# Kernel optimization log

Measured on AMD Instinct MI355X. Metric: run time of the kernel, lower is better.

The kernel has to match this reference:

```python
import jax, jax.numpy as jnp
import numpy as np

B, S, D = 4, 1024, 4096
HQ, HKV, HD = 32, 8, 128
N_REP = HQ // HKV


def _rope(x, cos, sin):
    # x: [b, s, h, hd]; cos/sin: [s, hd//2]; pairs are (x[..., 2i], x[..., 2i+1])
    xr = x[..., 0::2]
    xi = x[..., 1::2]
    c = cos[None, :, None, :]
    s = sin[None, :, None, :]
    out_r = xr * c - xi * s
    out_i = xr * s + xi * c
    return jnp.stack([out_r, out_i], axis=-1).reshape(x.shape)


def setup_inputs() -> dict:
    key = jax.random.key(0)
    ks = jax.random.split(key, 6)
    x = jax.random.normal(ks[0], (B, S, D), dtype=jnp.float32)
    wq = jax.random.normal(ks[1], (HQ * HD, D), dtype=jnp.float32) * 0.02
    wk = jax.random.normal(ks[2], (HKV * HD, D), dtype=jnp.float32) * 0.02
    wv = jax.random.normal(ks[3], (HKV * HD, D), dtype=jnp.float32) * 0.02
    wo = jax.random.normal(ks[4], (D, HQ * HD), dtype=jnp.float32) * 0.02
    # standard rotary frequencies, theta=10000
    inv_freq = 1.0 / (10000.0 ** (np.arange(0, HD, 2, dtype=np.float32) / HD))
    angles = np.outer(np.arange(S, dtype=np.float32), inv_freq)  # [S, HD//2]
    freqs_cos = jnp.asarray(np.cos(angles), dtype=jnp.float32)
    freqs_sin = jnp.asarray(np.sin(angles), dtype=jnp.float32)
    cache_k = jnp.zeros((B, S, HKV, HD), dtype=jnp.float32)
    cache_v = jnp.zeros((B, S, HKV, HD), dtype=jnp.float32)
    return {"x": x, "wq": wq, "wk": wk, "wv": wv, "wo": wo,
            "freqs_cos": freqs_cos, "freqs_sin": freqs_sin,
            "cache_k": cache_k, "cache_v": cache_v, "start_pos": 0}


def reference(x, wq, wk, wv, wo, freqs_cos, freqs_sin, cache_k, cache_v, start_pos):
    b, s, _ = x.shape
    xq = jnp.einsum('bsd,od->bso', x, wq).reshape(b, s, HQ, HD)
    xk = jnp.einsum('bsd,od->bso', x, wk).reshape(b, s, HKV, HD)
    xv = jnp.einsum('bsd,od->bso', x, wv).reshape(b, s, HKV, HD)
    xq = _rope(xq, freqs_cos, freqs_sin)
    xk = _rope(xk, freqs_cos, freqs_sin)
    # KV-cache append (intended semantics: store keys/values)
    cache_k = jax.lax.dynamic_update_slice(cache_k, xk, (0, start_pos, 0, 0))
    cache_v = jax.lax.dynamic_update_slice(cache_v, xv, (0, start_pos, 0, 0))
    keys = cache_k[:, :start_pos + s]      # [b, kv, HKV, HD]
    values = cache_v[:, :start_pos + s]
    # GQA repeat_kv -> [b, kv, HQ, HD]
    keys = jnp.repeat(keys, N_REP, axis=2)
    values = jnp.repeat(values, N_REP, axis=2)
    scores = jnp.einsum('bqhd,bkhd->bhqk', xq, keys) / jnp.sqrt(jnp.float32(HD))
    probs = jax.nn.softmax(scores.astype(jnp.float32), axis=-1).astype(xq.dtype)
    out = jnp.einsum('bhqk,bkhd->bqhd', probs, values).reshape(b, s, HQ * HD)
    return jnp.einsum('bso,do->bsd', out, wo)
```

## Files before the change

### kernel.cpp

```cpp
#include <hip/hip_runtime.h>

typedef __bf16 bf16_t;
typedef __bf16 bf16x8 __attribute__((ext_vector_type(8)));
typedef __bf16 bf16x4 __attribute__((ext_vector_type(4)));
typedef float  f32x4  __attribute__((ext_vector_type(4)));
typedef unsigned u32x4 __attribute__((ext_vector_type(4)));

#define SEQ    1024
#define DMODEL 4096
#define NHQ    32
#define NHKV   8
#define HDIM   128

#define GLOAD_LDS16(g, l)                                                  \
    __builtin_amdgcn_global_load_lds(                                      \
        (const __attribute__((address_space(1))) unsigned int*)(g),        \
        (__attribute__((address_space(3))) unsigned int*)(l), 16, 0, 0)

__global__ __launch_bounds__(256)
void f2b(const float* __restrict__ in, bf16_t* __restrict__ out, int n8)
{
    int i = blockIdx.x * 256 + threadIdx.x;
    if (i >= n8) return;
    const float4* p = (const float4*)in + 2 * (size_t)i;
    float4 a = p[0], b = p[1];
    bf16x8 o;
    o[0] = (bf16_t)a.x; o[1] = (bf16_t)a.y; o[2] = (bf16_t)a.z; o[3] = (bf16_t)a.w;
    o[4] = (bf16_t)b.x; o[5] = (bf16_t)b.y; o[6] = (bf16_t)b.z; o[7] = (bf16_t)b.w;
    *((bf16x8*)out + i) = o;
}

#define MFMA_(a, b, c) __builtin_amdgcn_mfma_f32_16x16x32_bf16(a, b, c, 0, 0, 0)
#define BAR    __builtin_amdgcn_s_barrier()
#define SCB    __builtin_amdgcn_sched_barrier(0)
#define PRIO1  __builtin_amdgcn_s_setprio(1)
#define PRIO0  __builtin_amdgcn_s_setprio(0)
#define WVM4   do { asm volatile("s_waitcnt vmcnt(4)" ::: "memory"); SCB; } while (0)

#define SA(bufo, half, ktb)  do {                                          \
    const char* g_ = ((half) ? aS1 : aS0) + (ktb);                         \
    GLOAD_LDS16(g_,      sd + (bufo) + (half) * 8192);                     \
    GLOAD_LDS16(g_ + 64, sd + (bufo) + (half) * 8192 + 16384);             \
} while (0)
#define SB(bufo, half, ktb)  do {                                          \
    const char* g_ = ((half) ? bS1 : bS0) + (ktb);                         \
    GLOAD_LDS16(g_,      sd + (bufo) + 32768 + (half) * 8192);             \
    GLOAD_LDS16(g_ + 64, sd + (bufo) + 32768 + (half) * 8192 + 16384);     \
} while (0)
#define LDA(bufo, mh) do { _Pragma("unroll")                               \
    for (int j = 0; j < 4; ++j) {                                          \
        afq[j][0] = *(const bf16x8*)(lds + (bufo) + aRow + (mh)*4096 + j*1024);         \
        afq[j][1] = *(const bf16x8*)(lds + (bufo) + aRow + (mh)*4096 + j*1024 + 16384); \
    } } while (0)
#define LDB(bufo, nh, dst) do { _Pragma("unroll")                          \
    for (int n2 = 0; n2 < 2; ++n2) {                                       \
        dst[n2][0] = *(const bf16x8*)(lds + (bufo) + bRow + (nh)*2048 + n2*1024);         \
        dst[n2][1] = *(const bf16x8*)(lds + (bufo) + bRow + (nh)*2048 + n2*1024 + 16384); \
    } } while (0)
#define MMQ(mlo, bfx, nlo) do { _Pragma("unroll")                          \
    for (int j = 0; j < 4; ++j) {                                          \
        acc[(mlo)+j][(nlo)  ] = MFMA_(afq[j][0], bfx[0][0], acc[(mlo)+j][(nlo)  ]); \
        acc[(mlo)+j][(nlo)  ] = MFMA_(afq[j][1], bfx[0][1], acc[(mlo)+j][(nlo)  ]); \
        acc[(mlo)+j][(nlo)+1] = MFMA_(afq[j][0], bfx[1][0], acc[(mlo)+j][(nlo)+1]); \
        acc[(mlo)+j][(nlo)+1] = MFMA_(afq[j][1], bfx[1][1], acc[(mlo)+j][(nlo)+1]); \
    } } while (0)

template<bool OUT_F32>
__global__ __launch_bounds__(512, 2)
void gemm256(const bf16_t* __restrict__ A, const bf16_t* __restrict__ B,
             void* __restrict__ Cv, int M, int N, int K, int nbn)
{
    __shared__ __align__(16) char lds[131072];

    const int nwg = gridDim.x;
    const int bid0 = blockIdx.x;
    const int bid = (bid0 & 7) * (nwg >> 3) + (bid0 >> 3);
    const int bm = bid / nbn, bn = bid % nbn;
    const int t = threadIdx.x;
    const int lane = t & 63, wid = t >> 6;
    const int wm = wid >> 2, wn = wid & 3;
    const int l15 = lane & 15, lg = lane >> 4;
    const int m0 = bm * 256, n0 = bn * 256;

    const int Krb = K * 2;
    const int srow = t >> 2;
    const int schunk = (((t & 3) ^ ((t >> 3) & 3)) << 4);
    const char* aS0 = (const char*)A + (size_t)(m0 + srow) * Krb + schunk;
    const char* aS1 = (const char*)A + (size_t)(m0 + 128 + srow) * Krb + schunk;
    const char* bS0 = (const char*)B + (size_t)(n0 + srow) * Krb + schunk;
    const char* bS1 = (const char*)B + (size_t)(n0 + 128 + srow) * Krb + schunk;
    char* sd = lds + t * 16;

    const int rchunk = ((lg ^ ((l15 >> 1) & 3)) << 4);
    const int aRow = (wm * 128 + l15) * 64 + rchunk;
    const int bRow = 32768 + (wn * 64 + l15) * 64 + rchunk;

    const int NT = K >> 6;
    f32x4 acc[8][4] = {};
    bf16x8 afq[4][2], bf0[2][2], bf1[2][2];

    SA(0, 0, 0); SA(0, 1, 0); SB(0, 0, 0); SB(0, 1, 0);
    SB(65536, 0, 128); SB(65536, 1, 128);
    WVM4;
    BAR;

    for (int T = 0; T < NT; T += 2) {
        const int k1 = (T + 1) * 128;
        const int k2 = (T + 2 < NT) ? (T + 2) * 128 : 0;
        const int k3 = (T + 3 < NT) ? (T + 3) * 128 : 0;
        LDA(0, 0); LDB(0, 0, bf0); SA(65536, 0, k1); BAR; SCB;
        PRIO1; MMQ(0, bf0, 0); PRIO0; BAR;
        LDB(0, 1, bf1); SA(65536, 1, k1); BAR; SCB;
        PRIO1; MMQ(0, bf1, 2); PRIO0; BAR;
        LDA(0, 1); SB(0, 0, k2); BAR; SCB;
        PRIO1; MMQ(4, bf1, 2); PRIO0; BAR;
        SB(0, 1, k2); BAR;
        PRIO1; MMQ(4, bf0, 0); PRIO0; WVM4; BAR;
        LDA(65536, 0); LDB(65536, 0, bf0); SA(0, 0, k2); BAR; SCB;
        PRIO1; MMQ(0, bf0, 0); PRIO0; BAR;
        LDB(65536, 1, bf1); SA(0, 1, k2); BAR; SCB;
        PRIO1; MMQ(0, bf1, 2); PRIO0; BAR;
        LDA(65536, 1); SB(65536, 0, k3); BAR; SCB;
        PRIO1; MMQ(4, bf1, 2); PRIO0; BAR;
        SB(65536, 1, k3); BAR;
        PRIO1; MMQ(4, bf0, 0); PRIO0; WVM4; BAR;
    }

    #pragma unroll
    for (int m = 0; m < 8; ++m) {
        int row0 = m0 + wm * 128 + m * 16 + lg * 4;
        #pragma unroll
        for (int n = 0; n < 4; ++n) {
            int col = n0 + wn * 64 + n * 16 + l15;
            #pragma unroll
            for (int i = 0; i < 4; ++i) {
                if constexpr (OUT_F32)
                    ((float*)Cv)[(size_t)(row0 + i) * N + col] = acc[m][n][i];
                else
                    ((bf16_t*)Cv)[(size_t)(row0 + i) * N + col] = (bf16_t)acc[m][n][i];
            }
        }
    }
}

template<int MODE>
__global__ __launch_bounds__(256, 4)
void gemm_bt(const bf16_t* __restrict__ A, const bf16_t* __restrict__ B,
             void* __restrict__ Cv, bf16_t* __restrict__ Vt,
             int M, int N, int K, int nbn)
{
    __shared__ __align__(16) bf16_t lA[128 * 32];
    __shared__ __align__(16) bf16_t lB[128 * 32];

    const int nwg = gridDim.x;
    const int bid0 = blockIdx.x;
    const int bid = (bid0 & 7) * (nwg >> 3) + (bid0 >> 3);
    const int bm = bid / nbn, bn = bid % nbn;
    const int t = threadIdx.x;
    const int lane = t & 63, wid = t >> 6;
    const int wrow = (wid >> 1) * 64, wcol = (wid & 1) * 64;
    const int l15 = lane & 15, lg = lane >> 4;
    const int m0 = bm * 128, n0 = bn * 128;

    const int r0 = t >> 2, pos0 = (t & 3) * 8;
    const int r1 = r0 + 64;

    const bf16_t* Ar0 = A + (size_t)(m0 + r0) * K + pos0;
    const bf16_t* Ar1 = A + (size_t)(m0 + r1) * K + pos0;
    const bf16_t* Br0 = B + (size_t)(n0 + r0) * K + pos0;
    const bf16_t* Br1 = B + (size_t)(n0 + r1) * K + pos0;

    f32x4 acc[4][4] = {};

    for (int k0 = 0; k0 < K; k0 += 32) {
        __syncthreads();
        GLOAD_LDS16(Ar0 + k0, lA + t * 8);
        GLOAD_LDS16(Ar1 + k0, lA + (t + 256) * 8);
        GLOAD_LDS16(Br0 + k0, lB + t * 8);
        GLOAD_LDS16(Br1 + k0, lB + (t + 256) * 8);
        __syncthreads();

        bf16x8 af[4], bfr[4];
        #pragma unroll
        for (int m = 0; m < 4; ++m)
            af[m] = *(const bf16x8*)(lA + (wrow + m * 16 + l15) * 32 + lg * 8);
        #pragma unroll
        for (int n = 0; n < 4; ++n)
            bfr[n] = *(const bf16x8*)(lB + (wcol + n * 16 + l15) * 32 + lg * 8);
        #pragma unroll
        for (int m = 0; m < 4; ++m)
            #pragma unroll
            for (int n = 0; n < 4; ++n)
                acc[m][n] = __builtin_amdgcn_mfma_f32_16x16x32_bf16(
                    af[m], bfr[n], acc[m][n], 0, 0, 0);
    }

    #pragma unroll
    for (int m = 0; m < 4; ++m) {
        #pragma unroll
        for (int n = 0; n < 4; ++n) {
            int col  = n0 + wcol + n * 16 + l15;
            int row0 = m0 + wrow + m * 16 + lg * 4;
            if constexpr (MODE == 0) {
                #pragma unroll
                for (int i = 0; i < 4; ++i)
                    ((bf16_t*)Cv)[(size_t)(row0 + i) * N + col] = (bf16_t)acc[m][n][i];
            } else if constexpr (MODE == 1) {
                #pragma unroll
                for (int i = 0; i < 4; ++i)
                    ((float*)Cv)[(size_t)(row0 + i) * N + col] = acc[m][n][i];
            } else {
                if (col < 1024) {
                    #pragma unroll
                    for (int i = 0; i < 4; ++i)
                        ((bf16_t*)Cv)[(size_t)(row0 + i) * 1024 + col] = (bf16_t)acc[m][n][i];
                } else {
                    bf16x4 pk;
                    #pragma unroll
                    for (int i = 0; i < 4; ++i) pk[i] = (bf16_t)acc[m][n][i];
                    *(bf16x4*)(Vt + (size_t)(col - 1024) * 4096 + row0) = pk;
                }
            }
        }
    }
}

__global__ __launch_bounds__(256)
void rope_kernel(bf16_t* __restrict__ X, const float* __restrict__ fc,
                 const float* __restrict__ fs, int nheads, int rowstride,
                 float oscale)
{
    int idx = blockIdx.x * 256 + threadIdx.x;
    int j4 = idx & 15;
    int rest = idx >> 4;
    int h = rest % nheads;
    int tok = rest / nheads;
    int s = tok & (SEQ - 1);
    bf16_t* p = X + (size_t)tok * rowstride + h * HDIM + j4 * 8;
    bf16x8 v = *(const bf16x8*)p;
    float4 c  = *(const float4*)(fc + s * 64 + j4 * 4);
    float4 sn = *(const float4*)(fs + s * 64 + j4 * 4);
    c.x *= oscale; c.y *= oscale; c.z *= oscale; c.w *= oscale;
    sn.x *= oscale; sn.y *= oscale; sn.z *= oscale; sn.w *= oscale;
    bf16x8 o;
    o[0] = (bf16_t)((float)v[0] * c.x - (float)v[1] * sn.x);
    o[1] = (bf16_t)((float)v[0] * sn.x + (float)v[1] * c.x);
    o[2] = (bf16_t)((float)v[2] * c.y - (float)v[3] * sn.y);
    o[3] = (bf16_t)((float)v[2] * sn.y + (float)v[3] * c.y);
    o[4] = (bf16_t)((float)v[4] * c.z - (float)v[5] * sn.z);
    o[5] = (bf16_t)((float)v[4] * sn.z + (float)v[5] * c.z);
    o[6] = (bf16_t)((float)v[6] * c.w - (float)v[7] * sn.w);
    o[7] = (bf16_t)((float)v[6] * sn.w + (float)v[7] * c.w);
    *(bf16x8*)p = o;
}

__global__ __launch_bounds__(512, 2)
void attn_kernel(const bf16_t* __restrict__ Q, const bf16_t* __restrict__ Kg,
                 const bf16_t* __restrict__ Vtg, bf16_t* __restrict__ O)
{
    __shared__ __align__(16) char klds[2][64 * 256];
    __shared__ __align__(16) char vlds[2][128 * 128];

    const int nwg = gridDim.x;
    const int bid0 = blockIdx.x;
    const int blk = (bid0 & 7) * (nwg >> 3) + (bid0 >> 3);
    const int qt = blk & 7;
    const int bh = blk >> 3;
    const int b = bh >> 5, h = bh & 31, kv = h >> 2;
    const int t = threadIdx.x, lane = t & 63, wid = t >> 6;
    const int l15 = lane & 15, lg = lane >> 4;
    const int swzk = (l15 & 7) << 4;

    const int qrow = qt * 128 + wid * 16 + l15;
    const size_t qbase = (size_t)(b * SEQ + qrow) * DMODEL + h * HDIM;
    bf16x8 qf[4];
    #pragma unroll
    for (int dc = 0; dc < 4; ++dc)
        qf[dc] = *(const bf16x8*)(Q + qbase + dc * 32 + lg * 8);

    const char* kgb = (const char*)Kg + ((size_t)(b * SEQ) * 1024 + kv * HDIM) * 2;
    const char* vgb = (const char*)Vtg + ((size_t)(kv * HDIM) * 4096 + b * SEQ) * 2;

    const int ck0 = t, ck1 = t + 512;
    const int kr0 = ck0 >> 4, kr1 = ck1 >> 4;
    const int kg0 = ((kr0 >> 5) << 5) + (((((kr0 & 15) >> 2) ^ ((kr0 >> 4) & 1)) << 3))
                  + (((kr0 >> 4) & 1) << 2) + (kr0 & 3);
    const int kg1 = ((kr1 >> 5) << 5) + (((((kr1 & 15) >> 2) ^ ((kr1 >> 4) & 1)) << 3))
                  + (((kr1 >> 4) & 1) << 2) + (kr1 & 3);
    const int kf0 = kg0 * 2048 + ((((ck0 & 15) << 4)) ^ ((kr0 & 7) << 4));
    const int kf1 = kg1 * 2048 + ((((ck1 & 15) << 4)) ^ ((kr1 & 7) << 4));
    const int vd0 = ck0 >> 3, vf0 = vd0 * 8192 + ((((ck0 & 7) << 4)) ^ ((vd0 & 7) << 4));
    const int vd1 = ck1 >> 3, vf1 = vd1 * 8192 + ((((ck1 & 7) << 4)) ^ ((vd1 & 7) << 4));

    f32x4 o[8] = {};
    float lrun = 0.f;

#define STAGE_KV(kt_, bi_) do {                                            \
    GLOAD_LDS16(kgb + (size_t)(kt_) * 131072 + kf0, klds[bi_] + ck0 * 16); \
    GLOAD_LDS16(kgb + (size_t)(kt_) * 131072 + kf1, klds[bi_] + ck1 * 16); \
    GLOAD_LDS16(vgb + (kt_) * 128 + vf0, vlds[bi_] + ck0 * 16);            \
    GLOAD_LDS16(vgb + (kt_) * 128 + vf1, vlds[bi_] + ck1 * 16);            \
} while (0)

    STAGE_KV(0, 0);
    __syncthreads();

    for (int kt = 0; kt < 16; ++kt) {
        const int cur = kt & 1;
        const int knx = (kt + 1 < 16) ? kt + 1 : 15;
        STAGE_KV(knx, cur ^ 1);

        f32x4 sacc[4] = {};
        #pragma unroll
        for (int kb = 0; kb < 4; ++kb) {
            const char* krow = klds[cur] + (kb * 16 + l15) * 256;
            #pragma unroll
            for (int dc = 0; dc < 4; ++dc) {
                bf16x8 kf = *(const bf16x8*)(krow + ((dc * 64 + lg * 16) ^ swzk));
                sacc[kb] = __builtin_amdgcn_mfma_f32_16x16x32_bf16(
                    kf, qf[dc], sacc[kb], 0, 0, 0);
            }
        }

        float ts = 0.f;
        unsigned qpk[4][2];
        #pragma unroll
        for (int kb = 0; kb < 4; ++kb) {
            float p0 = exp2f(sacc[kb][0] - 20.0f);
            float p1 = exp2f(sacc[kb][1] - 20.0f);
            float p2 = exp2f(sacc[kb][2] - 20.0f);
            float p3 = exp2f(sacc[kb][3] - 20.0f);
            ts += (p0 + p1) + (p2 + p3);
            asm("v_cvt_pk_bf16_f32 %0, %1, %2" : "=v"(qpk[kb][0]) : "v"(p0), "v"(p1));
            asm("v_cvt_pk_bf16_f32 %0, %1, %2" : "=v"(qpk[kb][1]) : "v"(p2), "v"(p3));
        }
        lrun += ts;

        #pragma unroll
        for (int c = 0; c < 2; ++c) {
            unsigned s0 = (unsigned)__shfl_xor((int)qpk[2 * c + 1][0], 16);
            unsigned s1 = (unsigned)__shfl_xor((int)qpk[2 * c + 1][1], 16);
            u32x4 w;
            w[0] = qpk[2 * c][0]; w[1] = qpk[2 * c][1]; w[2] = s0; w[3] = s1;
            bf16x8 a32 = __builtin_bit_cast(bf16x8, w);
            #pragma unroll
            for (int db = 0; db < 8; ++db) {
                int d = l15 + 16 * db;
                const char* va = vlds[cur] + d * 128 + ((c * 64 + lg * 16) ^ swzk);
                bf16x8 vf = *(const bf16x8*)va;
                o[db] = __builtin_amdgcn_mfma_f32_16x16x32_bf16(
                    a32, vf, o[db], 0, 0, 0);
            }
        }

        __syncthreads();
    }
#undef STAGE_KV

    lrun += __shfl_xor(lrun, 16);
    lrun += __shfl_xor(lrun, 32);

    #pragma unroll
    for (int i = 0; i < 4; ++i) {
        float li = __shfl(lrun, lg * 4 + i);
        float inv = 1.0f / li;
        int row = b * SEQ + qt * 128 + wid * 16 + lg * 4 + i;
        #pragma unroll
        for (int db = 0; db < 8; ++db) {
            int col = h * HDIM + l15 + 16 * db;
            O[(size_t)row * DMODEL + col] = (bf16_t)(o[db][i] * inv);
        }
    }
}

extern "C" void kernel_launch(void* const* d_in, const int* in_sizes, int n_in,
                              void* d_out, int out_size, void* d_ws, size_t ws_size,
                              hipStream_t stream)
{
    const float* x  = (const float*)d_in[0];
    const float* wq = (const float*)d_in[1];
    const float* wk = (const float*)d_in[2];
    const float* wv = (const float*)d_in[3];
    const float* wo = (const float*)d_in[4];
    const float* fc = (const float*)d_in[5];
    const float* fs = (const float*)d_in[6];

    const size_t T = (size_t)4096;
    bf16_t* Qw   = (bf16_t*)d_ws;
    bf16_t* Kw2  = Qw   + T * 4096;
    bf16_t* Vt   = Kw2  + T * 1024;
    bf16_t* AO   = Vt   + T * 1024;
    bf16_t* xb   = AO   + T * 4096;
    bf16_t* wqb  = xb   + T * 4096;
    bf16_t* wkvb = wqb  + T * 4096;
    bf16_t* wob  = wkvb + T * 2048;

    f2b<<<8192, 256, 0, stream>>>(x,  xb,  4096 * 4096 / 8);
    f2b<<<8192, 256, 0, stream>>>(wq, wqb, 4096 * 4096 / 8);
    f2b<<<2048, 256, 0, stream>>>(wk, wkvb,                       1024 * 4096 / 8);
    f2b<<<2048, 256, 0, stream>>>(wv, wkvb + (size_t)1024 * 4096, 1024 * 4096 / 8);
    f2b<<<8192, 256, 0, stream>>>(wo, wob, 4096 * 4096 / 8);

    gemm256<false><<<256, 512, 0, stream>>>(xb, wqb, Qw, 4096, 4096, 4096, 16);
    gemm_bt<2><<<512, 256, 0, stream>>>(xb, wkvb, Kw2, Vt, 4096, 2048, 4096, 16);

    rope_kernel<<<8192, 256, 0, stream>>>(Qw,  fc, fs, NHQ,  4096,
                                          0.08838834764831845f * 1.4426950408889634f);
    rope_kernel<<<2048, 256, 0, stream>>>(Kw2, fc, fs, NHKV, 1024, 1.0f);

    attn_kernel<<<1024, 512, 0, stream>>>(Qw, Kw2, Vt, AO);

    gemm256<true><<<256, 512, 0, stream>>>(AO, wob, d_out, 4096, 4096, 4096, 16);
}
```

Baseline: 482.8 us.

## Software-pipeline LDS fragment reads with inline asm and explicit lgkmcnt waits

Rewrites the GEMM main loop so LDS-to-register fragment loads use inline-asm ds_read_b128 with explicit lgkmcnt waits. Each load is issued one phase ahead of the MFMAs that consume it, using double-buffered A and B fragment registers. This removes one barrier per phase and relaxes the vmcnt wait, so LDS reads overlap MFMA work. It raises register pressure and relies on hand-counted waitcnt values, where a miscount gives a race or wrong results.

```diff
diff --git a/kernel.cpp b/kernel.cpp
--- a/kernel.cpp
+++ b/kernel.cpp
@@ -35,7 +35,25 @@
 #define SCB    __builtin_amdgcn_sched_barrier(0)
 #define PRIO1  __builtin_amdgcn_s_setprio(1)
 #define PRIO0  __builtin_amdgcn_s_setprio(0)
-#define WVM4   do { asm volatile("s_waitcnt vmcnt(4)" ::: "memory"); SCB; } while (0)
+#define WVM2   do { asm volatile("s_waitcnt vmcnt(2)" ::: "memory"); SCB; } while (0)
+#define WLGK(N) do { asm volatile("s_waitcnt lgkmcnt(" N ")" ::: "memory"); SCB; } while (0)
+#define BC8(x) __builtin_bit_cast(bf16x8, x)
+
+#define DSR(dst, a, OFF) \
+    asm volatile("ds_read_b128 %0, %1 offset:" OFF : "=v"(dst) : "v"(a))
+
+#define LDA_ASM(DST, bufo, mh) do {                                        \
+    unsigned aA_ = aBase + (bufo) + (mh) * 4096;                           \
+    DSR(DST[0][0], aA_, "0");     DSR(DST[0][1], aA_, "16384");            \
+    DSR(DST[1][0], aA_, "1024");  DSR(DST[1][1], aA_, "17408");            \
+    DSR(DST[2][0], aA_, "2048");  DSR(DST[2][1], aA_, "18432");            \
+    DSR(DST[3][0], aA_, "3072");  DSR(DST[3][1], aA_, "19456");            \
+} while (0)
+#define LDB_ASM(DST, bufo, nh) do {                                        \
+    unsigned bA_ = bBase + (bufo) + (nh) * 2048;                           \
+    DSR(DST[0][0], bA_, "0");     DSR(DST[0][1], bA_, "16384");            \
+    DSR(DST[1][0], bA_, "1024");  DSR(DST[1][1], bA_, "17408");            \
+} while (0)
 
 #define SA(bufo, half, ktb)  do {                                          \
     const char* g_ = ((half) ? aS1 : aS0) + (ktb);                         \
@@ -47,22 +65,13 @@
     GLOAD_LDS16(g_,      sd + (bufo) + 32768 + (half) * 8192);             \
     GLOAD_LDS16(g_ + 64, sd + (bufo) + 32768 + (half) * 8192 + 16384);     \
 } while (0)
-#define LDA(bufo, mh) do { _Pragma("unroll")                               \
+
+#define MMQ2(mlo, AFS, BFS, nlo) do { _Pragma("unroll")                    \
     for (int j = 0; j < 4; ++j) {                                          \
-        afq[j][0] = *(const bf16x8*)(lds + (bufo) + aRow + (mh)*4096 + j*1024);         \
-        afq[j][1] = *(const bf16x8*)(lds + (bufo) + aRow + (mh)*4096 + j*1024 + 16384); \
-    } } while (0)
-#define LDB(bufo, nh, dst) do { _Pragma("unroll")                          \
-    for (int n2 = 0; n2 < 2; ++n2) {                                       \
-        dst[n2][0] = *(const bf16x8*)(lds + (bufo) + bRow + (nh)*2048 + n2*1024);         \
-        dst[n2][1] = *(const bf16x8*)(lds + (bufo) + bRow + (nh)*2048 + n2*1024 + 16384); \
-    } } while (0)
-#define MMQ(mlo, bfx, nlo) do { _Pragma("unroll")                          \
-    for (int j = 0; j < 4; ++j) {                                          \
-        acc[(mlo)+j][(nlo)  ] = MFMA_(afq[j][0], bfx[0][0], acc[(mlo)+j][(nlo)  ]); \
-        acc[(mlo)+j][(nlo)  ] = MFMA_(afq[j][1], bfx[0][1], acc[(mlo)+j][(nlo)  ]); \
-        acc[(mlo)+j][(nlo)+1] = MFMA_(afq[j][0], bfx[1][0], acc[(mlo)+j][(nlo)+1]); \
-        acc[(mlo)+j][(nlo)+1] = MFMA_(afq[j][1], bfx[1][1], acc[(mlo)+j][(nlo)+1]); \
+        acc[(mlo)+j][(nlo)  ] = MFMA_(BC8(AFS[j][0]), BC8(BFS[0][0]), acc[(mlo)+j][(nlo)  ]); \
+        acc[(mlo)+j][(nlo)  ] = MFMA_(BC8(AFS[j][1]), BC8(BFS[0][1]), acc[(mlo)+j][(nlo)  ]); \
+        acc[(mlo)+j][(nlo)+1] = MFMA_(BC8(AFS[j][0]), BC8(BFS[1][0]), acc[(mlo)+j][(nlo)+1]); \
+        acc[(mlo)+j][(nlo)+1] = MFMA_(BC8(AFS[j][1]), BC8(BFS[1][1]), acc[(mlo)+j][(nlo)+1]); \
     } } while (0)
 
 template<bool OUT_F32>
@@ -92,38 +101,64 @@
     char* sd = lds + t * 16;
 
     const int rchunk = ((lg ^ ((l15 >> 1) & 3)) << 4);
-    const int aRow = (wm * 128 + l15) * 64 + rchunk;
-    const int bRow = 32768 + (wn * 64 + l15) * 64 + rchunk;
+    const unsigned ldsW = (unsigned)(size_t)lds;
+    const unsigned aBase = ldsW + (unsigned)((wm * 128 + l15) * 64 + rchunk);
+    const unsigned bBase = ldsW + (unsigned)(32768 + (wn * 64 + l15) * 64 + rchunk);
 
     const int NT = K >> 6;
     f32x4 acc[8][4] = {};
-    bf16x8 afq[4][2], bf0[2][2], bf1[2][2];
+    f32x4 afX[4][2], afY[4][2], b0A[2][2], b0B[2][2], b1[2][2];
 
     SA(0, 0, 0); SA(0, 1, 0); SB(0, 0, 0); SB(0, 1, 0);
     SB(65536, 0, 128); SB(65536, 1, 128);
-    WVM4;
+    asm volatile("s_waitcnt vmcnt(4)" ::: "memory"); SCB;
     BAR;
+    LDA_ASM(afX, 0, 0); LDB_ASM(b0A, 0, 0);
 
     for (int T = 0; T < NT; T += 2) {
         const int k1 = (T + 1) * 128;
         const int k2 = (T + 2 < NT) ? (T + 2) * 128 : 0;
         const int k3 = (T + 3 < NT) ? (T + 3) * 128 : 0;
-        LDA(0, 0); LDB(0, 0, bf0); SA(65536, 0, k1); BAR; SCB;
-        PRIO1; MMQ(0, bf0, 0); PRIO0; BAR;
-        LDB(0, 1, bf1); SA(65536, 1, k1); BAR; SCB;
-        PRIO1; MMQ(0, bf1, 2); PRIO0; BAR;
-        LDA(0, 1); SB(0, 0, k2); BAR; SCB;
-        PRIO1; MMQ(4, bf1, 2); PRIO0; BAR;
-        SB(0, 1, k2); BAR;
-        PRIO1; MMQ(4, bf0, 0); PRIO0; WVM4; BAR;
-        LDA(65536, 0); LDB(65536, 0, bf0); SA(0, 0, k2); BAR; SCB;
-        PRIO1; MMQ(0, bf0, 0); PRIO0; BAR;
-        LDB(65536, 1, bf1); SA(0, 1, k2); BAR; SCB;
-        PRIO1; MMQ(0, bf1, 2); PRIO0; BAR;
-        LDA(65536, 1); SB(65536, 0, k3); BAR; SCB;
-        PRIO1; MMQ(4, bf1, 2); PRIO0; BAR;
-        SB(65536, 1, k3); BAR;
-        PRIO1; MMQ(4, bf0, 0); PRIO0; WVM4; BAR;
+        BAR;
+        LDB_ASM(b1, 0, 1);
+        SA(65536, 0, k1);
+        WLGK("4");
+        PRIO1; MMQ2(0, afX, b0A, 0); PRIO0; SCB;
+        BAR;
+        LDA_ASM(afY, 0, 1);
+        SA(65536, 1, k1);
+        WLGK("8");
+        PRIO1; MMQ2(0, afX, b1, 2); PRIO0; SCB;
+        BAR;
+        SB(0, 0, k2);
+        WLGK("0");
+        PRIO1; MMQ2(4, afY, b1, 2); PRIO0;
+        WVM2;
+        BAR;
+        LDA_ASM(afX, 65536, 0); LDB_ASM(b0B, 65536, 0);
+        SB(0, 1, k2);
+        WLGK("12");
+        PRIO1; MMQ2(4, afY, b0A, 0); PRIO0; SCB;
+        BAR;
+        LDB_ASM(b1, 65536, 1);
+        SA(0, 0, k2);
+        WLGK("4");
+        PRIO1; MMQ2(0, afX, b0B, 0); PRIO0; SCB;
+        BAR;
+        LDA_ASM(afY, 65536, 1);
+        SA(0, 1, k2);
+        WLGK("8");
+        PRIO1; MMQ2(0, afX, b1, 2); PRIO0; SCB;
+        BAR;
+        SB(65536, 0, k3);
+        WLGK("0");
+        PRIO1; MMQ2(4, afY, b1, 2); PRIO0;
+        WVM2;
+        BAR;
+        LDA_ASM(afX, 0, 0); LDB_ASM(b0A, 0, 0);
+        SB(65536, 1, k3);
+        WLGK("12");
+        PRIO1; MMQ2(4, afY, b0B, 0); PRIO0; SCB;
     }
 
     #pragma unroll
```

After: 495.2 us. 2.6% more time.

## Add 256x128-tile double-buffered GEMM kernel for the Q projection

Applied to the files above, without the earlier changes.

Introduces a new gemm_mn kernel with 256x128 output tiles, K-step 32, double-buffered LDS filled via global_load_lds, XOR-swizzled LDS layout and an XCD-aware block remap. It replaces the existing gemm256 launch for the Q projection, doubling the grid to 512 workgroups and asking for higher occupancy (launch bounds of 4 blocks). The goal is better CU utilization and latency hiding on the 4096^3 GEMM. The trade-off is less reuse per tile and a barrier on every short K step, and the epilogue writes scalar outputs instead of vectorized ones.

```diff
diff --git a/kernel.cpp b/kernel.cpp
--- a/kernel.cpp
+++ b/kernel.cpp
@@ -36,6 +36,86 @@
 #define PRIO1  __builtin_amdgcn_s_setprio(1)
 #define PRIO0  __builtin_amdgcn_s_setprio(0)
 #define WVM4   do { asm volatile("s_waitcnt vmcnt(4)" ::: "memory"); SCB; } while (0)
+
+#define STG2(b_, ktb) do {                                                 \
+    GLOAD_LDS16(aS + (ktb),             ldsA[b_] + t * 16);                \
+    GLOAD_LDS16(aS + 128 * Krb + (ktb), ldsA[b_] + 8192 + t * 16);         \
+    GLOAD_LDS16(bS + (ktb),             ldsB[b_] + t * 16);                \
+} while (0)
+
+template<bool OUT_F32>
+__global__ __launch_bounds__(512, 4)
+void gemm_mn(const bf16_t* __restrict__ A, const bf16_t* __restrict__ B,
+             void* __restrict__ Cv, int M, int N, int K, int nbn)
+{
+    __shared__ __align__(16) char ldsA[2][16384];
+    __shared__ __align__(16) char ldsB[2][8192];
+
+    const int nwg = gridDim.x;
+    const int bid0 = blockIdx.x;
+    const int bid = (bid0 & 7) * (nwg >> 3) + (bid0 >> 3);
+    const int bm = bid / nbn, bn = bid % nbn;
+    const int t = threadIdx.x;
+    const int lane = t & 63, wid = t >> 6;
+    const int wm = wid >> 1, wn = wid & 1;
+    const int l15 = lane & 15, lg = lane >> 4;
+    const int m0 = bm * 256, n0 = bn * 128;
+
+    const int Krb = K * 2;
+    const int srow = t >> 2;
+    const int scol0 = (((t & 3) ^ ((srow >> 1) & 3)) << 4);
+    const char* aS = (const char*)A + (size_t)(m0 + srow) * Krb + scol0;
+    const char* bS = (const char*)B + (size_t)(n0 + srow) * Krb + scol0;
+
+    const int rchunk = ((lg ^ ((l15 >> 1) & 3)) << 4);
+    const int aRow = (wm * 64 + l15) * 64 + rchunk;
+    const int bRow = (wn * 64 + l15) * 64 + rchunk;
+
+    const int NT = K >> 5;
+    f32x4 acc[4][4] = {};
+
+    STG2(0, 0);
+    __syncthreads();
+
+    for (int tt = 0; tt < NT; ++tt) {
+        const int buf = tt & 1;
+        const int ks = (tt + 1 < NT) ? (tt + 1) * 64 : 0;
+        STG2(buf ^ 1, ks);
+
+        bf16x8 af[4], bf[4];
+        #pragma unroll
+        for (int m = 0; m < 4; ++m)
+            af[m] = *(const bf16x8*)(ldsA[buf] + aRow + m * 1024);
+        #pragma unroll
+        for (int n = 0; n < 4; ++n)
+            bf[n] = *(const bf16x8*)(ldsB[buf] + bRow + n * 1024);
+        PRIO1;
+        #pragma unroll
+        for (int m = 0; m < 4; ++m)
+            #pragma unroll
+            for (int n = 0; n < 4; ++n)
+                acc[m][n] = MFMA_(af[m], bf[n], acc[m][n]);
+        PRIO0;
+
+        __syncthreads();
+    }
+
+    #pragma unroll
+    for (int m = 0; m < 4; ++m) {
+        int row0 = m0 + wm * 64 + m * 16 + lg * 4;
+        #pragma unroll
+        for (int n = 0; n < 4; ++n) {
+            int col = n0 + wn * 64 + n * 16 + l15;
+            #pragma unroll
+            for (int i = 0; i < 4; ++i) {
+                if constexpr (OUT_F32)
+                    ((float*)Cv)[(size_t)(row0 + i) * N + col] = acc[m][n][i];
+                else
+                    ((bf16_t*)Cv)[(size_t)(row0 + i) * N + col] = (bf16_t)acc[m][n][i];
+            }
+        }
+    }
+}
 
 #define SA(bufo, half, ktb)  do {                                          \
     const char* g_ = ((half) ? aS1 : aS0) + (ktb);                         \
@@ -401,7 +481,7 @@
     f2b<<<2048, 256, 0, stream>>>(wv, wkvb + (size_t)1024 * 4096, 1024 * 4096 / 8);
     f2b<<<8192, 256, 0, stream>>>(wo, wob, 4096 * 4096 / 8);
 
-    gemm256<false><<<256, 512, 0, stream>>>(xb, wqb, Qw, 4096, 4096, 4096, 16);
+    gemm_mn<false><<<512, 512, 0, stream>>>(xb, wqb, Qw, 4096, 4096, 4096, 32);
     gemm_bt<2><<<512, 256, 0, stream>>>(xb, wkvb, Kw2, Vt, 4096, 2048, 4096, 16);
 
     rope_kernel<<<8192, 256, 0, stream>>>(Qw,  fc, fs, NHQ,  4096,
```

Measured after the change: 526.8 us. +9.1%, slower.
